# Kernel optimization log

Measured on AMD Instinct MI355X. Metric: run time of the kernel, lower is better.

The kernel has to match this reference:

```python
import jax, jax.numpy as jnp
import numpy as np

ALL_WINDOW_SIZES = [1, 2, 4, 8, 16, 32]
ATTENTION_WINDOW = 32
T, D, N = 8192, 128, 4096
NW = len(ALL_WINDOW_SIZES)


def _layernorm(x, g, b, eps=1e-5):
    mu = x.mean(axis=-1, keepdims=True)
    var = ((x - mu) ** 2).mean(axis=-1, keepdims=True)
    return (x - mu) / jnp.sqrt(var + eps) * g + b


def setup_inputs() -> dict:
    key = jax.random.key(0)
    ks = jax.random.split(key, 16)
    s = 0.02
    return {
        "inputEmbeds": jax.random.normal(ks[0], (T, D), dtype=jnp.float32),
        # per-neuron weights stacked -> Linear(D, N)
        "neuronW": jax.random.normal(ks[1], (D, N), dtype=jnp.float32) * s,
        "neuronB": jnp.zeros((N,), dtype=jnp.float32),
        # tiny attention layer (single head, Q/K/V projections)
        "Wq": jax.random.normal(ks[2], (D, D), dtype=jnp.float32) * s,
        "bq": jnp.zeros((D,), dtype=jnp.float32),
        "Wk": jax.random.normal(ks[3], (D, D), dtype=jnp.float32) * s,
        "bk": jnp.zeros((D,), dtype=jnp.float32),
        "Wv": jax.random.normal(ks[4], (D, D), dtype=jnp.float32) * s,
        "bv": jnp.zeros((D,), dtype=jnp.float32),
        # attentionProjection = LayerNorm(D) -> Linear(D, N)
        "ln_g": jnp.ones((D,), dtype=jnp.float32),
        "ln_b": jnp.zeros((D,), dtype=jnp.float32),
        "projW": jax.random.normal(ks[5], (D, N), dtype=jnp.float32) * s,
        "projb": jnp.zeros((N,), dtype=jnp.float32),
        "windowWeighting": jnp.ones((NW,), dtype=jnp.float32),
        # combinationLayer: Linear(N*NW, N)
        "comboW": jax.random.normal(ks[6], (N * NW, N), dtype=jnp.float32) * 0.005,
        "combob": jnp.zeros((N,), dtype=jnp.float32),
    }


def _tiny_attn(x, Wq, bq, Wk, bk, Wv, bv):
    # x: [B, W, D] -> single-head self attention
    q = x @ Wq + bq
    k = x @ Wk + bk
    v = x @ Wv + bv
    scores = jnp.einsum("bqd,bkd->bqk", q, k) / jnp.sqrt(jnp.asarray(x.shape[-1], x.dtype))
    return jnp.einsum("bqk,bkd->bqd", jax.nn.softmax(scores, axis=-1), v)


def reference(inputEmbeds, neuronW, neuronB, Wq, bq, Wk, bk, Wv, bv,
              ln_g, ln_b, projW, projb, windowWeighting, comboW, combob):
    # all neurons over all tokens: [T, N], tanh activation, clamp to [-5, 5]
    acts = jnp.clip(jnp.tanh(inputEmbeds @ neuronW + neuronB), -5.0, 5.0)

    window_means = []
    for w in ALL_WINDOW_SIZES:
        if w == ATTENTION_WINDOW:
            xw = inputEmbeds[-w:][None]  # [1, w, D]
            attended = _tiny_attn(xw, Wq, bq, Wk, bk, Wv, bv)  # [1, w, D]
            attn_mean = attended.mean(axis=1)  # [1, D]
            proj = _layernorm(attn_mean, ln_g, ln_b) @ projW + projb  # [1, N]
            window_means.append(proj)
        else:
            window_means.append(acts[-w:].mean(axis=0, keepdims=True))  # [1, N]

    norm_w = (windowWeighting + 0.1) / (windowWeighting.sum() + 0.1)
    weighted = jnp.concatenate(
        [window_means[i] * norm_w[i] for i in range(NW)], axis=1)  # [1, N*NW]
    return weighted @ comboW + combob  # [1, N]
```

## Files before the change

### kernel.cpp

```cpp
#include <hip/hip_runtime.h>

#define T_TOK 8192
#define D_DIM 128
#define N_NEU 4096
#define RPC 48
#define NCHUNK 512
#define NPART NCHUNK

typedef float f4_t __attribute__((ext_vector_type(4)));

struct SmemActs {
    float xs16[16][128];
    float wst[32][256];
};
struct SmemQkv {
    float xs[32][128];
    float w[128][128];
};
union SmemA {
    SmemActs a;
    SmemQkv q;
};

__global__ void acts_qkv_kernel(
    const float* __restrict__ x,
    const float* __restrict__ neuronW, const float* __restrict__ neuronB,
    const float* __restrict__ Wq, const float* __restrict__ bq,
    const float* __restrict__ Wk, const float* __restrict__ bk,
    const float* __restrict__ Wv, const float* __restrict__ bv,
    float* __restrict__ means,
    float* __restrict__ qkv)
{
    __shared__ SmemA sm;
    const int tid = threadIdx.x;
    const int bid = blockIdx.x;

    if (bid < 16) {
        const int n0 = bid * 256;
        const int n = n0 + tid;
        for (int idx = tid; idx < 16 * 128; idx += 256) {
            int t = idx >> 7, d = idx & 127;
            sm.a.xs16[t][d] = x[(size_t)(T_TOK - 16 + t) * D_DIM + d];
        }
        float acc[16];
        float bias = neuronB[n];
#pragma unroll
        for (int t = 0; t < 16; ++t) acc[t] = bias;
        const f4_t* W4 = reinterpret_cast<const f4_t*>(neuronW);
        f4_t* wst4 = reinterpret_cast<f4_t*>(&sm.a.wst[0][0]);
        for (int c = 0; c < 4; ++c) {
            const int d0 = c * 32;
            __syncthreads();
#pragma unroll
            for (int k = 0; k < 8; ++k) {
                int idx = tid + k * 256;
                int dd = idx >> 6, j4 = idx & 63;
                wst4[dd * 64 + j4] = W4[(size_t)(d0 + dd) * 1024 + (n0 >> 2) + j4];
            }
            __syncthreads();
#pragma unroll
            for (int dd = 0; dd < 32; ++dd) {
                float w = sm.a.wst[dd][tid];
#pragma unroll
                for (int t = 0; t < 16; ++t) acc[t] += sm.a.xs16[t][d0 + dd] * w;
            }
        }
#pragma unroll
        for (int t = 0; t < 16; ++t) acc[t] = tanhf(acc[t]);
        float s1 = acc[15];
        float s2 = s1 + acc[14];
        float s4 = s2 + acc[13] + acc[12];
        float s8 = s4 + acc[11] + acc[10] + acc[9] + acc[8];
        float s16 = s8 + acc[7] + acc[6] + acc[5] + acc[4] + acc[3] + acc[2] + acc[1] + acc[0];
        means[0 * N_NEU + n] = s1;
        means[1 * N_NEU + n] = s2 * 0.5f;
        means[2 * N_NEU + n] = s4 * 0.25f;
        means[3 * N_NEU + n] = s8 * 0.125f;
        means[4 * N_NEU + n] = s16 * 0.0625f;
        return;
    }

    const int m = bid - 16;
    const float* Wm = (m == 0) ? Wq : ((m == 1) ? Wk : Wv);
    const float* bb = (m == 0) ? bq : ((m == 1) ? bk : bv);

    f4_t* xs4 = reinterpret_cast<f4_t*>(&sm.q.xs[0][0]);
    const f4_t* X4 = reinterpret_cast<const f4_t*>(x + (size_t)(T_TOK - 32) * D_DIM);
#pragma unroll
    for (int k = 0; k < 4; ++k) xs4[tid + k * 256] = X4[tid + k * 256];
    f4_t* w4 = reinterpret_cast<f4_t*>(&sm.q.w[0][0]);
    const f4_t* Wm4 = reinterpret_cast<const f4_t*>(Wm);
#pragma unroll
    for (int k = 0; k < 16; ++k) w4[tid + k * 256] = Wm4[tid + k * 256];
    __syncthreads();

    const int d = tid & 127;
    const int g = tid >> 7;
    float acc[16];
    float bias = bb[d];
#pragma unroll
    for (int i = 0; i < 16; ++i) acc[i] = bias;
#pragma unroll 4
    for (int e = 0; e < 128; ++e) {
        float w = sm.q.w[e][d];
#pragma unroll
        for (int i = 0; i < 16; ++i) acc[i] += sm.q.xs[g * 16 + i][e] * w;
    }
#pragma unroll
    for (int i = 0; i < 16; ++i) qkv[m * 4096 + (g * 16 + i) * 128 + d] = acc[i];
}

struct SmemAttn {
    float qs[32][128];
    float kt[128][33];
    float vs[32][128];
    float ps[32][33];
    float pbar[32];
    float mvec[128];
    float red[2];
};

__global__ void attn_kernel(const float* __restrict__ qkv,
                            const float* __restrict__ ln_g, const float* __restrict__ ln_b,
                            float* __restrict__ yvec)
{
    __shared__ SmemAttn sm;
    const int tid = threadIdx.x;
    for (int idx = tid; idx < 32 * 128; idx += 256) {
        int i = idx >> 7, d = idx & 127;
        sm.qs[i][d] = qkv[idx];
        sm.kt[d][i] = qkv[4096 + idx];
        sm.vs[i][d] = qkv[8192 + idx];
    }
    __syncthreads();
    const float scale = 0.08838834764831845f;
#pragma unroll
    for (int rep = 0; rep < 4; ++rep) {
        int idx = tid + rep * 256;
        int i = idx >> 5, j = idx & 31;
        float acc = 0.f;
        for (int e = 0; e < 128; ++e) acc += sm.qs[i][e] * sm.kt[e][j];
        sm.ps[i][j] = acc * scale;
    }
    __syncthreads();
    if (tid < 32) {
        float mx = -1e30f;
        for (int j = 0; j < 32; ++j) mx = fmaxf(mx, sm.ps[tid][j]);
        float s = 0.f;
        for (int j = 0; j < 32; ++j) { float e = expf(sm.ps[tid][j] - mx); sm.ps[tid][j] = e; s += e; }
        float inv = 1.f / s;
        for (int j = 0; j < 32; ++j) sm.ps[tid][j] *= inv;
    }
    __syncthreads();
    if (tid < 32) {
        float s = 0.f;
        for (int i = 0; i < 32; ++i) s += sm.ps[i][tid];
        sm.pbar[tid] = s * (1.f / 32.f);
    }
    __syncthreads();
    if (tid < 128) {
        float s = 0.f;
        for (int j = 0; j < 32; ++j) s += sm.pbar[j] * sm.vs[j][tid];
        sm.mvec[tid] = s;
    }
    __syncthreads();
    if (tid < 64) {
        float p = sm.mvec[tid] + sm.mvec[tid + 64];
        for (int off = 32; off; off >>= 1) p += __shfl_down(p, off);
        if (tid == 0) sm.red[0] = p * (1.f / 128.f);
    }
    __syncthreads();
    float mu = sm.red[0];
    if (tid < 64) {
        float t1 = sm.mvec[tid] - mu, t2 = sm.mvec[tid + 64] - mu;
        float p = t1 * t1 + t2 * t2;
        for (int off = 32; off; off >>= 1) p += __shfl_down(p, off);
        if (tid == 0) sm.red[1] = rsqrtf(p * (1.f / 128.f) + 1e-5f);
    }
    __syncthreads();
    if (tid < 128) {
        yvec[tid] = (sm.mvec[tid] - mu) * sm.red[1] * ln_g[tid] + ln_b[tid];
    }
}

struct SmemV {
    float ys[128];
    float wst[32][256];
};

__global__ void build_v_kernel(const float* __restrict__ yvec,
                               const float* __restrict__ projW,
                               const float* __restrict__ projb,
                               const float* __restrict__ ww,
                               const float* __restrict__ means,
                               float* __restrict__ v)
{
    __shared__ SmemV sm;
    const int tid = threadIdx.x;
    const int n0 = blockIdx.x * 256;
    const int n = n0 + tid;

    if (tid < 128) sm.ys[tid] = yvec[tid];
    float denom = 0.1f;
#pragma unroll
    for (int i = 0; i < 6; ++i) denom += ww[i];
    const float inv = 1.f / denom;

    float acc = projb[n];
    const f4_t* P4 = reinterpret_cast<const f4_t*>(projW);
    f4_t* wst4 = reinterpret_cast<f4_t*>(&sm.wst[0][0]);
    for (int c = 0; c < 4; ++c) {
        const int d0 = c * 32;
        __syncthreads();
#pragma unroll
        for (int k = 0; k < 8; ++k) {
            int idx = tid + k * 256;
            int dd = idx >> 6, j4 = idx & 63;
            wst4[dd * 64 + j4] = P4[(size_t)(d0 + dd) * 1024 + (n0 >> 2) + j4];
        }
        __syncthreads();
#pragma unroll
        for (int dd = 0; dd < 32; ++dd) {
            acc += sm.ys[d0 + dd] * sm.wst[dd][tid];
        }
    }
#pragma unroll
    for (int s = 0; s < 5; ++s)
        v[s * N_NEU + n] = means[s * N_NEU + n] * ((ww[s] + 0.1f) * inv);
    v[5 * N_NEU + n] = acc * ((ww[5] + 0.1f) * inv);
}

__global__ __launch_bounds__(256) void combo_partial_kernel(
    const float* __restrict__ v,
    const float* __restrict__ comboW,
    float* __restrict__ part)
{
    __shared__ float vsm[RPC];
    const int tid = threadIdx.x;
    const int chunk = blockIdx.x >> 2;
    const int cb = blockIdx.x & 3;
    const int row0 = chunk * RPC;

    if (tid < RPC) vsm[tid] = v[row0 + tid];
    __syncthreads();

    const f4_t* W4 = reinterpret_cast<const f4_t*>(comboW);
    const size_t base = (size_t)row0 * 1024 + cb * 256 + tid;
    f4_t acc = {0.f, 0.f, 0.f, 0.f};
#pragma unroll 8
    for (int r = 0; r < RPC; ++r) {
        acc += W4[base + (size_t)r * 1024] * vsm[r];
    }
    reinterpret_cast<f4_t*>(part)[(size_t)chunk * 1024 + cb * 256 + tid] = acc;
}

__global__ void combo_reduce_kernel(const float* __restrict__ part,
                                    const float* __restrict__ bias,
                                    float* __restrict__ out)
{
    __shared__ f4_t red[4][64];
    const int tid = threadIdx.x;
    const int h = tid >> 6;
    const int j = tid & 63;
    const int n4 = blockIdx.x * 64 + j;
    const f4_t* P4 = reinterpret_cast<const f4_t*>(part);
    f4_t acc = {0.f, 0.f, 0.f, 0.f};
#pragma unroll 8
    for (int c = h * 128; c < h * 128 + 128; ++c)
        acc += P4[(size_t)c * 1024 + n4];
    red[h][j] = acc;
    __syncthreads();
    if (h == 0) {
        f4_t s = red[0][j] + red[1][j] + red[2][j] + red[3][j];
        s += reinterpret_cast<const f4_t*>(bias)[n4];
        reinterpret_cast<f4_t*>(out)[n4] = s;
    }
}

extern "C" void kernel_launch(void* const* d_in, const int* in_sizes, int n_in,
                              void* d_out, int out_size, void* d_ws, size_t ws_size,
                              hipStream_t stream) {
    const float* inputEmbeds = (const float*)d_in[0];
    const float* neuronW     = (const float*)d_in[1];
    const float* neuronB     = (const float*)d_in[2];
    const float* Wq          = (const float*)d_in[3];
    const float* bq          = (const float*)d_in[4];
    const float* Wk          = (const float*)d_in[5];
    const float* bk          = (const float*)d_in[6];
    const float* Wv          = (const float*)d_in[7];
    const float* bv          = (const float*)d_in[8];
    const float* ln_g        = (const float*)d_in[9];
    const float* ln_b        = (const float*)d_in[10];
    const float* projW       = (const float*)d_in[11];
    const float* projb       = (const float*)d_in[12];
    const float* ww          = (const float*)d_in[13];
    const float* comboW      = (const float*)d_in[14];
    const float* combob      = (const float*)d_in[15];
    float* out = (float*)d_out;
    float* ws  = (float*)d_ws;

    float* means = ws;
    float* yvec  = ws + 20480;
    float* qkv   = ws + 20608;
    float* v     = ws + 32896;
    float* part  = ws + 57472;

    acts_qkv_kernel<<<19, 256, 0, stream>>>(inputEmbeds, neuronW, neuronB,
                                            Wq, bq, Wk, bk, Wv, bv, means, qkv);
    attn_kernel<<<1, 256, 0, stream>>>(qkv, ln_g, ln_b, yvec);
    build_v_kernel<<<16, 256, 0, stream>>>(yvec, projW, projb, ww, means, v);
    combo_partial_kernel<<<NCHUNK * 4, 256, 0, stream>>>(v, comboW, part);
    combo_reduce_kernel<<<16, 256, 0, stream>>>(part, combob, out);
}
```

Baseline: 130.9 us.

## Fuse attention into projection kernel, write weighted v directly, enlarge combo chunks

Merges the single-block attention kernel with the projection/v-building kernel, so each of the 16 blocks recomputes the tiny attention redundantly, and one launch plus the yvec round trip are removed. The activation kernel now writes window-weighted v directly instead of an intermediate means buffer. The combo partial kernel processes 192 rows per chunk across 128 chunks with nontemporal loads of comboW, which shrinks the partial buffer and the reduce work. The costs are redundant attention compute and fewer blocks streaming the large comboW matrix.

```diff
diff --git a/kernel.cpp b/kernel.cpp
--- a/kernel.cpp
+++ b/kernel.cpp
@@ -3,9 +3,8 @@
 #define T_TOK 8192
 #define D_DIM 128
 #define N_NEU 4096
-#define RPC 48
-#define NCHUNK 512
-#define NPART NCHUNK
+#define RPC 192
+#define NCHUNK 128
 
 typedef float f4_t __attribute__((ext_vector_type(4)));
 
@@ -28,7 +27,8 @@
     const float* __restrict__ Wq, const float* __restrict__ bq,
     const float* __restrict__ Wk, const float* __restrict__ bk,
     const float* __restrict__ Wv, const float* __restrict__ bv,
-    float* __restrict__ means,
+    const float* __restrict__ ww,
+    float* __restrict__ v,
     float* __restrict__ qkv)
 {
     __shared__ SmemA sm;
@@ -67,16 +67,20 @@
         }
 #pragma unroll
         for (int t = 0; t < 16; ++t) acc[t] = tanhf(acc[t]);
+        float denom = 0.1f;
+#pragma unroll
+        for (int i = 0; i < 6; ++i) denom += ww[i];
+        const float inv = 1.f / denom;
         float s1 = acc[15];
         float s2 = s1 + acc[14];
         float s4 = s2 + acc[13] + acc[12];
         float s8 = s4 + acc[11] + acc[10] + acc[9] + acc[8];
         float s16 = s8 + acc[7] + acc[6] + acc[5] + acc[4] + acc[3] + acc[2] + acc[1] + acc[0];
-        means[0 * N_NEU + n] = s1;
-        means[1 * N_NEU + n] = s2 * 0.5f;
-        means[2 * N_NEU + n] = s4 * 0.25f;
-        means[3 * N_NEU + n] = s8 * 0.125f;
-        means[4 * N_NEU + n] = s16 * 0.0625f;
+        v[0 * N_NEU + n] = s1 * ((ww[0] + 0.1f) * inv);
+        v[1 * N_NEU + n] = s2 * 0.5f * ((ww[1] + 0.1f) * inv);
+        v[2 * N_NEU + n] = s4 * 0.25f * ((ww[2] + 0.1f) * inv);
+        v[3 * N_NEU + n] = s8 * 0.125f * ((ww[3] + 0.1f) * inv);
+        v[4 * N_NEU + n] = s16 * 0.0625f * ((ww[4] + 0.1f) * inv);
         return;
     }
 
@@ -110,27 +114,40 @@
     for (int i = 0; i < 16; ++i) qkv[m * 4096 + (g * 16 + i) * 128 + d] = acc[i];
 }
 
-struct SmemAttn {
-    float qs[32][128];
-    float kt[128][33];
-    float vs[32][128];
-    float ps[32][33];
-    float pbar[32];
-    float mvec[128];
-    float red[2];
+struct SmemAP {
+    union {
+        struct {
+            float qs[32][128];
+            float kt[128][33];
+            float vs[32][128];
+            float ps[32][33];
+            float pbar[32];
+            float mvec[128];
+            float red[2];
+        } a;
+        struct {
+            float wst[32][256];
+        } p;
+    } u;
+    float ys[128];
 };
 
-__global__ void attn_kernel(const float* __restrict__ qkv,
-                            const float* __restrict__ ln_g, const float* __restrict__ ln_b,
-                            float* __restrict__ yvec)
+__global__ void attn_proj_kernel(
+    const float* __restrict__ qkv,
+    const float* __restrict__ ln_g, const float* __restrict__ ln_b,
+    const float* __restrict__ projW,
+    const float* __restrict__ projb,
+    const float* __restrict__ ww,
+    float* __restrict__ v)
 {
-    __shared__ SmemAttn sm;
+    __shared__ SmemAP sm;
     const int tid = threadIdx.x;
+
     for (int idx = tid; idx < 32 * 128; idx += 256) {
         int i = idx >> 7, d = idx & 127;
-        sm.qs[i][d] = qkv[idx];
-        sm.kt[d][i] = qkv[4096 + idx];
-        sm.vs[i][d] = qkv[8192 + idx];
+        sm.u.a.qs[i][d] = qkv[idx];
+        sm.u.a.kt[d][i] = qkv[4096 + idx];
+        sm.u.a.vs[i][d] = qkv[8192 + idx];
     }
     __syncthreads();
     const float scale = 0.08838834764831845f;
@@ -139,76 +156,60 @@
         int idx = tid + rep * 256;
         int i = idx >> 5, j = idx & 31;
         float acc = 0.f;
-        for (int e = 0; e < 128; ++e) acc += sm.qs[i][e] * sm.kt[e][j];
-        sm.ps[i][j] = acc * scale;
+        for (int e = 0; e < 128; ++e) acc += sm.u.a.qs[i][e] * sm.u.a.kt[e][j];
+        sm.u.a.ps[i][j] = acc * scale;
     }
     __syncthreads();
     if (tid < 32) {
         float mx = -1e30f;
-        for (int j = 0; j < 32; ++j) mx = fmaxf(mx, sm.ps[tid][j]);
+        for (int j = 0; j < 32; ++j) mx = fmaxf(mx, sm.u.a.ps[tid][j]);
         float s = 0.f;
-        for (int j = 0; j < 32; ++j) { float e = expf(sm.ps[tid][j] - mx); sm.ps[tid][j] = e; s += e; }
+        for (int j = 0; j < 32; ++j) { float e = expf(sm.u.a.ps[tid][j] - mx); sm.u.a.ps[tid][j] = e; s += e; }
         float inv = 1.f / s;
-        for (int j = 0; j < 32; ++j) sm.ps[tid][j] *= inv;
+        for (int j = 0; j < 32; ++j) sm.u.a.ps[tid][j] *= inv;
     }
     __syncthreads();
     if (tid < 32) {
         float s = 0.f;
-        for (int i = 0; i < 32; ++i) s += sm.ps[i][tid];
-        sm.pbar[tid] = s * (1.f / 32.f);
+        for (int i = 0; i < 32; ++i) s += sm.u.a.ps[i][tid];
+        sm.u.a.pbar[tid] = s * (1.f / 32.f);
     }
     __syncthreads();
     if (tid < 128) {
         float s = 0.f;
-        for (int j = 0; j < 32; ++j) s += sm.pbar[j] * sm.vs[j][tid];
-        sm.mvec[tid] = s;
+        for (int j = 0; j < 32; ++j) s += sm.u.a.pbar[j] * sm.u.a.vs[j][tid];
+        sm.u.a.mvec[tid] = s;
     }
     __syncthreads();
     if (tid < 64) {
-        float p = sm.mvec[tid] + sm.mvec[tid + 64];
+        float p = sm.u.a.mvec[tid] + sm.u.a.mvec[tid + 64];
         for (int off = 32; off; off >>= 1) p += __shfl_down(p, off);
-        if (tid == 0) sm.red[0] = p * (1.f / 128.f);
-    }
-    __syncthreads();
-    float mu = sm.red[0];
+        if (tid == 0) sm.u.a.red[0] = p * (1.f / 128.f);
+    }
+    __syncthreads();
+    float mu = sm.u.a.red[0];
     if (tid < 64) {
-        float t1 = sm.mvec[tid] - mu, t2 = sm.mvec[tid + 64] - mu;
+        float t1 = sm.u.a.mvec[tid] - mu, t2 = sm.u.a.mvec[tid + 64] - mu;
         float p = t1 * t1 + t2 * t2;
         for (int off = 32; off; off >>= 1) p += __shfl_down(p, off);
-        if (tid == 0) sm.red[1] = rsqrtf(p * (1.f / 128.f) + 1e-5f);
+        if (tid == 0) sm.u.a.red[1] = rsqrtf(p * (1.f / 128.f) + 1e-5f);
     }
     __syncthreads();
     if (tid < 128) {
-        yvec[tid] = (sm.mvec[tid] - mu) * sm.red[1] * ln_g[tid] + ln_b[tid];
-    }
-}
-
-struct SmemV {
-    float ys[128];
-    float wst[32][256];
-};
-
-__global__ void build_v_kernel(const float* __restrict__ yvec,
-                               const float* __restrict__ projW,
-                               const float* __restrict__ projb,
-                               const float* __restrict__ ww,
-                               const float* __restrict__ means,
-                               float* __restrict__ v)
-{
-    __shared__ SmemV sm;
-    const int tid = threadIdx.x;
+        sm.ys[tid] = (sm.u.a.mvec[tid] - mu) * sm.u.a.red[1] * ln_g[tid] + ln_b[tid];
+    }
+    __syncthreads();
+
     const int n0 = blockIdx.x * 256;
     const int n = n0 + tid;
-
-    if (tid < 128) sm.ys[tid] = yvec[tid];
     float denom = 0.1f;
 #pragma unroll
     for (int i = 0; i < 6; ++i) denom += ww[i];
-    const float inv = 1.f / denom;
+    const float nw5 = (ww[5] + 0.1f) / denom;
 
     float acc = projb[n];
     const f4_t* P4 = reinterpret_cast<const f4_t*>(projW);
-    f4_t* wst4 = reinterpret_cast<f4_t*>(&sm.wst[0][0]);
+    f4_t* wst4 = reinterpret_cast<f4_t*>(&sm.u.p.wst[0][0]);
     for (int c = 0; c < 4; ++c) {
         const int d0 = c * 32;
         __syncthreads();
@@ -221,13 +222,10 @@
         __syncthreads();
 #pragma unroll
         for (int dd = 0; dd < 32; ++dd) {
-            acc += sm.ys[d0 + dd] * sm.wst[dd][tid];
+            acc += sm.ys[d0 + dd] * sm.u.p.wst[dd][tid];
         }
     }
-#pragma unroll
-    for (int s = 0; s < 5; ++s)
-        v[s * N_NEU + n] = means[s * N_NEU + n] * ((ww[s] + 0.1f) * inv);
-    v[5 * N_NEU + n] = acc * ((ww[5] + 0.1f) * inv);
+    v[5 * N_NEU + n] = acc * nw5;
 }
 
 __global__ __launch_bounds__(256) void combo_partial_kernel(
@@ -249,7 +247,8 @@
     f4_t acc = {0.f, 0.f, 0.f, 0.f};
 #pragma unroll 8
     for (int r = 0; r < RPC; ++r) {
-        acc += W4[base + (size_t)r * 1024] * vsm[r];
+        f4_t w = __builtin_nontemporal_load(&W4[base + (size_t)r * 1024]);
+        acc += w * vsm[r];
     }
     reinterpret_cast<f4_t*>(part)[(size_t)chunk * 1024 + cb * 256 + tid] = acc;
 }
@@ -266,7 +265,7 @@
     const f4_t* P4 = reinterpret_cast<const f4_t*>(part);
     f4_t acc = {0.f, 0.f, 0.f, 0.f};
 #pragma unroll 8
-    for (int c = h * 128; c < h * 128 + 128; ++c)
+    for (int c = h * 32; c < h * 32 + 32; ++c)
         acc += P4[(size_t)c * 1024 + n4];
     red[h][j] = acc;
     __syncthreads();
@@ -299,16 +298,13 @@
     float* out = (float*)d_out;
     float* ws  = (float*)d_ws;
 
-    float* means = ws;
-    float* yvec  = ws + 20480;
-    float* qkv   = ws + 20608;
-    float* v     = ws + 32896;
-    float* part  = ws + 57472;
+    float* v    = ws;
+    float* qkv  = ws + 24576;
+    float* part = ws + 36864;
 
     acts_qkv_kernel<<<19, 256, 0, stream>>>(inputEmbeds, neuronW, neuronB,
-                                            Wq, bq, Wk, bk, Wv, bv, means, qkv);
-    attn_kernel<<<1, 256, 0, stream>>>(qkv, ln_g, ln_b, yvec);
-    build_v_kernel<<<16, 256, 0, stream>>>(yvec, projW, projb, ww, means, v);
+                                            Wq, bq, Wk, bk, Wv, bv, ww, v, qkv);
+    attn_proj_kernel<<<16, 256, 0, stream>>>(qkv, ln_g, ln_b, projW, projb, ww, v);
     combo_partial_kernel<<<NCHUNK * 4, 256, 0, stream>>>(v, comboW, part);
     combo_reduce_kernel<<<16, 256, 0, stream>>>(part, combob, out);
 }
```

After: 109.1 us. -16.7%, faster.
